# Optimization experiments

Measured on AMD Instinct MI355X. Metric: run time of the kernel, lower is better.

## Reference

```python
import jax, jax.numpy as jnp
import numpy as np

HEADS = 8
DIM_HEAD = 32
SCALE = DIM_HEAD ** -0.5


def setup_inputs() -> dict:
    key = jax.random.key(0)
    k1, k2, k3 = jax.random.split(key, 3)
    B, H, W, C = 16, 64, 64, 256
    hidden = HEADS * DIM_HEAD  # 256
    x = jax.random.normal(k1, (B, H, W, C), dtype=jnp.float32)
    # 1x1 convs with no bias == dense matmuls over channel dim (glorot-ish scale)
    w_qkv = jax.random.normal(k2, (C, 3 * hidden), dtype=jnp.float32) * (1.0 / np.sqrt(C))
    w_out = jax.random.normal(k3, (hidden, C), dtype=jnp.float32) * (1.0 / np.sqrt(hidden))
    return {"x": x, "w_qkv": w_qkv, "w_out": w_out}


def reference(x, w_qkv, w_out):
    B, H, W, C = x.shape
    n = H * W
    # to_qkv: 1x1 conv, no bias
    qkv = jnp.einsum('bhwc,cf->bhwf', x, w_qkv)  # [B,H,W,3*hidden]
    q, k, v = jnp.split(qkv, 3, axis=-1)

    def to_heads(t):
        # 'b x y (h c) -> b h c (x y)'
        t = t.reshape(B, n, HEADS, DIM_HEAD)
        return jnp.transpose(t, (0, 2, 3, 1))  # [B, heads, dim_head, n]

    q, k, v = to_heads(q), to_heads(k), to_heads(v)
    q = jax.nn.softmax(q, axis=-2) * SCALE      # softmax over feature dim d
    k = jax.nn.softmax(k, axis=-1)              # softmax over spatial dim n
    context = jnp.einsum('bhdn,bhen->bhde', k, v)   # [B, heads, d, e]
    out = jnp.einsum('bhde,bhdn->bhen', context, q)  # [B, heads, e, n]
    # 'b h c (x y) -> b x y (h c)'
    out = jnp.transpose(out, (0, 3, 1, 2)).reshape(B, H, W, HEADS * DIM_HEAD)
    # to_out: 1x1 conv, no bias
    return jnp.einsum('bhwf,fc->bhwc', out, w_out)
```

## Files before the change

kernel.cpp:

```cpp
#include <hip/hip_runtime.h>

using short8 = __attribute__((ext_vector_type(8))) short;
using f32x4  = __attribute__((ext_vector_type(4))) float;

#define SCALE_Q 0.17677669529663687f
#define NCHUNK 16

__device__ __forceinline__ unsigned short f2bf(float f) {
  unsigned u = __float_as_uint(f);
  return (unsigned short)((u + 0x7FFFu + ((u >> 16) & 1u)) >> 16);
}
__device__ __forceinline__ float bf2f(unsigned h) { return __uint_as_float(h << 16); }

__device__ __forceinline__ void bf8_to_f(uint4 r, float* o) {
  o[0] = bf2f(r.x & 0xffffu); o[1] = bf2f(r.x >> 16);
  o[2] = bf2f(r.y & 0xffffu); o[3] = bf2f(r.y >> 16);
  o[4] = bf2f(r.z & 0xffffu); o[5] = bf2f(r.z >> 16);
  o[6] = bf2f(r.w & 0xffffu); o[7] = bf2f(r.w >> 16);
}

__global__ __launch_bounds__(256) void prep_kernel(
    const float* __restrict__ x, const float* __restrict__ wqkv, const float* __restrict__ wout,
    unsigned short* __restrict__ xb, unsigned short* __restrict__ wqkvT,
    unsigned short* __restrict__ woutT) {
  const int blk = blockIdx.x;
  if (blk < 16384) {
    const size_t i = ((size_t)blk * 256 + threadIdx.x) * 4;
    const float4 v = *(const float4*)(x + i);
    *(ushort4*)(xb + i) = make_ushort4(f2bf(v.x), f2bf(v.y), f2bf(v.z), f2bf(v.w));
  } else if (blk < 16384 + 768) {
    const int n = blk - 16384, k = threadIdx.x;
    wqkvT[n * 256 + k] = f2bf(wqkv[(size_t)k * 768 + n]);
  } else {
    const int c = blk - 16384 - 768, f = threadIdx.x;
    woutT[c * 256 + f] = f2bf(wout[(size_t)f * 256 + c]);
  }
}

__global__ __launch_bounds__(256) void gemm_qkv(
    const unsigned short* __restrict__ A, const unsigned short* __restrict__ BT,
    unsigned short* __restrict__ KV, unsigned short* __restrict__ QS, int K) {
  __shared__ unsigned short As[2][128][40];
  __shared__ unsigned short Bs[2][128][40];
  const int cpx = (int)gridDim.x >> 3;
  const int lin = ((int)blockIdx.x & 7) * cpx + ((int)blockIdx.x >> 3);
  const int bn = lin % 6, bm = lin / 6;
  const int tid = threadIdx.x, lane = tid & 63, wid = tid >> 6;
  const int wr = wid >> 1, wc = wid & 1;
  const int fr = lane & 15, hi = lane >> 4, fk = hi * 8;
  f32x4 acc[4][4] = {};
  const size_t abase = (size_t)bm * 128 * K;
  const size_t bbase = (size_t)bn * 128 * K;

  const int srow = tid >> 2, skc = (tid & 3) * 8;
  uint4 ra0, ra1, rb0, rb1;
  const unsigned short* Ap = A + abase + (size_t)srow * K + skc;
  const unsigned short* Bp = BT + bbase + (size_t)srow * K + skc;

  ra0 = *(const uint4*)(Ap);            ra1 = *(const uint4*)(Ap + (size_t)64 * K);
  rb0 = *(const uint4*)(Bp);            rb1 = *(const uint4*)(Bp + (size_t)64 * K);
  *(uint4*)&As[0][srow][skc] = ra0;     *(uint4*)&As[0][srow + 64][skc] = ra1;
  *(uint4*)&Bs[0][srow][skc] = rb0;     *(uint4*)&Bs[0][srow + 64][skc] = rb1;
  __syncthreads();

  const int ktiles = K >> 5;
  int cur = 0;
  for (int t = 0; t < ktiles; ++t) {
    if (t + 1 < ktiles) {
      const int kt = (t + 1) * 32;
      ra0 = *(const uint4*)(Ap + kt);     ra1 = *(const uint4*)(Ap + (size_t)64 * K + kt);
      rb0 = *(const uint4*)(Bp + kt);     rb1 = *(const uint4*)(Bp + (size_t)64 * K + kt);
    }
    short8 af[4], bfv[4];
#pragma unroll
    for (int i = 0; i < 4; ++i) {
      af[i]  = *(const short8*)&As[cur][wr * 64 + i * 16 + fr][fk];
      bfv[i] = *(const short8*)&Bs[cur][wc * 64 + i * 16 + fr][fk];
    }
#pragma unroll
    for (int mi = 0; mi < 4; ++mi)
#pragma unroll
      for (int nj = 0; nj < 4; ++nj)
        acc[mi][nj] = __builtin_amdgcn_mfma_f32_16x16x32_bf16(bfv[nj], af[mi], acc[mi][nj], 0, 0, 0);
    if (t + 1 < ktiles) {
      *(uint4*)&As[cur ^ 1][srow][skc] = ra0;  *(uint4*)&As[cur ^ 1][srow + 64][skc] = ra1;
      *(uint4*)&Bs[cur ^ 1][srow][skc] = rb0;  *(uint4*)&Bs[cur ^ 1][srow + 64][skc] = rb1;
    }
    __syncthreads();
    cur ^= 1;
  }

  const size_t r0 = (size_t)bm * 128 + wr * 64;
  if (bn < 2) {
    const int c0 = bn * 128 + wc * 64;
#pragma unroll
    for (int mi = 0; mi < 4; ++mi) {
      const size_t row = r0 + mi * 16 + fr;
#pragma unroll
      for (int p = 0; p < 2; ++p) {
        const f32x4 a0 = acc[mi][2 * p], a1 = acc[mi][2 * p + 1];
        float mx = fmaxf(fmaxf(fmaxf(a0[0], a0[1]), fmaxf(a0[2], a0[3])),
                         fmaxf(fmaxf(a1[0], a1[1]), fmaxf(a1[2], a1[3])));
        mx = fmaxf(mx, __shfl_xor(mx, 16, 64));
        mx = fmaxf(mx, __shfl_xor(mx, 32, 64));
        float e0[4], e1[4], s = 0.f;
#pragma unroll
        for (int r = 0; r < 4; ++r) {
          e0[r] = __expf(a0[r] - mx); e1[r] = __expf(a1[r] - mx);
          s += e0[r] + e1[r];
        }
        s += __shfl_xor(s, 16, 64);
        s += __shfl_xor(s, 32, 64);
        const float inv = SCALE_Q / s;
        unsigned short* qp = QS + row * 256 + c0 + p * 32 + hi * 4;
        *(ushort4*)(qp)      = make_ushort4(f2bf(e0[0]*inv), f2bf(e0[1]*inv), f2bf(e0[2]*inv), f2bf(e0[3]*inv));
        *(ushort4*)(qp + 16) = make_ushort4(f2bf(e1[0]*inv), f2bf(e1[1]*inv), f2bf(e1[2]*inv), f2bf(e1[3]*inv));
      }
    }
    return;
  }
  const int colbase = (bn - 2) * 128 + wc * 64;
#pragma unroll
  for (int mi = 0; mi < 4; ++mi) {
    const size_t row = r0 + mi * 16 + fr;
#pragma unroll
    for (int nj = 0; nj < 4; ++nj) {
      const int col0 = colbase + nj * 16 + hi * 4;
      const f32x4 v = acc[mi][nj];
      *(ushort4*)(KV + row * 512 + col0) =
          make_ushort4(f2bf(v[0]), f2bf(v[1]), f2bf(v[2]), f2bf(v[3]));
    }
  }
}

__global__ __launch_bounds__(256) void gemm_out(
    const unsigned short* __restrict__ A, const unsigned short* __restrict__ BT,
    float* __restrict__ D, int K) {
  __shared__ unsigned short As[2][128][40];
  __shared__ unsigned short Bs[2][128][40];
  const int bn = blockIdx.x, bm = blockIdx.y, bz = blockIdx.z;
  const int tid = threadIdx.x, lane = tid & 63, wid = tid >> 6;
  const int wr = wid >> 1, wc = wid & 1;
  const int fr = lane & 15, hi = lane >> 4, fk = hi * 8;
  f32x4 acc[4][4] = {};
  const size_t abase = (size_t)bz * 4096 * 256 + (size_t)bm * 128 * K;
  const size_t bbase = (size_t)bz * 256 * 256 + (size_t)bn * 128 * K;

  const int srow = tid >> 2, skc = (tid & 3) * 8;
  uint4 ra0, ra1, rb0, rb1;
  const unsigned short* Ap = A + abase + (size_t)srow * K + skc;
  const unsigned short* Bp = BT + bbase + (size_t)srow * K + skc;

  ra0 = *(const uint4*)(Ap);            ra1 = *(const uint4*)(Ap + (size_t)64 * K);
  rb0 = *(const uint4*)(Bp);            rb1 = *(const uint4*)(Bp + (size_t)64 * K);
  *(uint4*)&As[0][srow][skc] = ra0;     *(uint4*)&As[0][srow + 64][skc] = ra1;
  *(uint4*)&Bs[0][srow][skc] = rb0;     *(uint4*)&Bs[0][srow + 64][skc] = rb1;
  __syncthreads();

  const int ktiles = K >> 5;
  int cur = 0;
  for (int t = 0; t < ktiles; ++t) {
    if (t + 1 < ktiles) {
      const int kt = (t + 1) * 32;
      ra0 = *(const uint4*)(Ap + kt);     ra1 = *(const uint4*)(Ap + (size_t)64 * K + kt);
      rb0 = *(const uint4*)(Bp + kt);     rb1 = *(const uint4*)(Bp + (size_t)64 * K + kt);
    }
    short8 af[4], bfv[4];
#pragma unroll
    for (int i = 0; i < 4; ++i) {
      af[i]  = *(const short8*)&As[cur][wr * 64 + i * 16 + fr][fk];
      bfv[i] = *(const short8*)&Bs[cur][wc * 64 + i * 16 + fr][fk];
    }
#pragma unroll
    for (int mi = 0; mi < 4; ++mi)
#pragma unroll
      for (int nj = 0; nj < 4; ++nj)
        acc[mi][nj] = __builtin_amdgcn_mfma_f32_16x16x32_bf16(bfv[nj], af[mi], acc[mi][nj], 0, 0, 0);
    if (t + 1 < ktiles) {
      *(uint4*)&As[cur ^ 1][srow][skc] = ra0;  *(uint4*)&As[cur ^ 1][srow + 64][skc] = ra1;
      *(uint4*)&Bs[cur ^ 1][srow][skc] = rb0;  *(uint4*)&Bs[cur ^ 1][srow + 64][skc] = rb1;
    }
    __syncthreads();
    cur ^= 1;
  }

  const size_t r0 = (size_t)bm * 128 + wr * 64;
  const int colbase = bn * 128 + wc * 64;
  float* Dz = D + (size_t)bz * 4096 * 256;
#pragma unroll
  for (int mi = 0; mi < 4; ++mi) {
    const size_t row = r0 + mi * 16 + fr;
#pragma unroll
    for (int nj = 0; nj < 4; ++nj) {
      const f32x4 v = acc[mi][nj];
      *(float4*)(Dz + row * 256 + colbase + nj * 16 + hi * 4) =
          make_float4(v[0], v[1], v[2], v[3]);
    }
  }
}

__global__ __launch_bounds__(256) void ctx_part_kernel(const unsigned short* __restrict__ kv,
                                                       float* __restrict__ part,
                                                       float* __restrict__ spart) {
  const int blk = blockIdx.x;
  const int bh = blk >> 4, chunk = blk & 15;
  const int b = bh >> 3, h = bh & 7;
  const int tid = threadIdx.x, d = tid & 31, g = tid >> 5;
  const unsigned short* kbase =
      kv + (size_t)b * 4096 * 512 + h * 32 + (size_t)chunk * 256 * 512;
  const unsigned short* vbase = kbase + 256;

  __shared__ float ek[64][36], vv[64][36];
  float a0 = 0.f, a1 = 0.f, a2 = 0.f, a3 = 0.f, ssum = 0.f;
  const int e0 = g * 4;
  const int sn = tid >> 2, sc = (tid & 3) * 8;
  const unsigned short* kp0 = kbase + (size_t)sn * 512 + sc;
  const unsigned short* vp0 = vbase + (size_t)sn * 512 + sc;
  uint4 kr = *(const uint4*)kp0;
  uint4 vr = *(const uint4*)vp0;
  for (int n0 = 0; n0 < 256; n0 += 64) {
    float kf[8], vf[8];
    bf8_to_f(kr, kf); bf8_to_f(vr, vf);
    uint4 krn = kr, vrn = vr;
    if (n0 + 64 < 256) {
      krn = *(const uint4*)(kp0 + (size_t)(n0 + 64) * 512);
      vrn = *(const uint4*)(vp0 + (size_t)(n0 + 64) * 512);
    }
#pragma unroll
    for (int j = 0; j < 8; ++j) { ek[sn][sc + j] = __expf(kf[j]); vv[sn][sc + j] = vf[j]; }
    __syncthreads();
#pragma unroll 8
    for (int i = 0; i < 64; ++i) {
      const float kd = ek[i][d];
      const float4 v4 = *(const float4*)&vv[i][e0];
      ssum += kd;
      a0 += kd * v4.x; a1 += kd * v4.y; a2 += kd * v4.z; a3 += kd * v4.w;
    }
    __syncthreads();
    kr = krn; vr = vrn;
  }
  float* pp = part + ((size_t)chunk * 128 + bh) * 1024 + d * 32 + e0;
  pp[0] = a0; pp[1] = a1; pp[2] = a2; pp[3] = a3;
  if (g == 0) spart[((size_t)chunk * 128 + bh) * 32 + d] = ssum;
}

__global__ __launch_bounds__(256) void ctx_combine_kernel(const float* __restrict__ part,
                                                          const float* __restrict__ spart,
                                                          float* __restrict__ ctx) {
  const int bh = blockIdx.x, tid = threadIdx.x;
  __shared__ float sinv[32];
  if (tid < 32) {
    float s = 0.f;
#pragma unroll
    for (int c = 0; c < NCHUNK; ++c) s += spart[((size_t)c * 128 + bh) * 32 + tid];
    sinv[tid] = 1.0f / s;
  }
  __syncthreads();
  float4 acc = make_float4(0.f, 0.f, 0.f, 0.f);
#pragma unroll
  for (int c = 0; c < NCHUNK; ++c) {
    const float4 p = *(const float4*)(part + ((size_t)c * 128 + bh) * 1024 + tid * 4);
    acc.x += p.x; acc.y += p.y; acc.z += p.z; acc.w += p.w;
  }
  const float si = sinv[tid >> 3];
  float4* cp = (float4*)(ctx + (size_t)bh * 1024 + tid * 4);
  *cp = make_float4(acc.x * si, acc.y * si, acc.z * si, acc.w * si);
}

__global__ __launch_bounds__(256) void w2_kernel(const float* __restrict__ ctx,
                                                 const unsigned short* __restrict__ woutT,
                                                 unsigned short* __restrict__ W2T) {
  const int b = blockIdx.x >> 4, cg = blockIdx.x & 15;
  const int tid = threadIdx.x;
  __shared__ float cs[8 * 32 * 32];
  {
    const float4* src = (const float4*)(ctx + (size_t)b * 8192);
    float4* dst = (float4*)cs;
#pragma unroll
    for (int i = 0; i < 8; ++i) dst[tid + i * 256] = src[tid + i * 256];
  }
  __syncthreads();
  const int c = cg * 16 + (tid >> 4), chunk = tid & 15;
  const int h = chunk >> 1, d0 = (chunk & 1) * 16;
  float wf[32];
  {
    const uint4* wp = (const uint4*)(woutT + (size_t)c * 256 + h * 32);
    bf8_to_f(wp[0], wf + 0); bf8_to_f(wp[1], wf + 8);
    bf8_to_f(wp[2], wf + 16); bf8_to_f(wp[3], wf + 24);
  }
  unsigned short o[16];
#pragma unroll
  for (int dd = 0; dd < 16; ++dd) {
    const float* cp = cs + h * 1024 + (d0 + dd) * 32;
    float acc = 0.f;
#pragma unroll
    for (int e = 0; e < 32; ++e) acc += cp[e] * wf[e];
    o[dd] = f2bf(acc);
  }
  uint4* op = (uint4*)(W2T + ((size_t)b * 256 + c) * 256 + chunk * 16);
  op[0] = make_uint4((unsigned)o[0] | ((unsigned)o[1] << 16), (unsigned)o[2] | ((unsigned)o[3] << 16),
                     (unsigned)o[4] | ((unsigned)o[5] << 16), (unsigned)o[6] | ((unsigned)o[7] << 16));
  op[1] = make_uint4((unsigned)o[8] | ((unsigned)o[9] << 16), (unsigned)o[10] | ((unsigned)o[11] << 16),
                     (unsigned)o[12] | ((unsigned)o[13] << 16), (unsigned)o[14] | ((unsigned)o[15] << 16));
}

extern "C" void kernel_launch(void* const* d_in, const int* in_sizes, int n_in,
                              void* d_out, int out_size, void* d_ws, size_t ws_size,
                              hipStream_t stream) {
  const float* x     = (const float*)d_in[0];
  const float* wqkv  = (const float*)d_in[1];
  const float* wout  = (const float*)d_in[2];
  float* out = (float*)d_out;

  char* ws = (char*)d_ws;
  unsigned short* xb    = (unsigned short*)(ws);
  unsigned short* wqkvT = (unsigned short*)(ws + 33554432);
  unsigned short* woutT = (unsigned short*)(ws + 33947648);
  unsigned short* kv    = (unsigned short*)(ws + 34078720);
  float*          ctx   = (float*)        (ws + 101187584);
  unsigned short* qs    = (unsigned short*)(ws + 101711872);
  float*          part  = (float*)(ws);
  float*          spart = (float*)(ws + 8388608);
  unsigned short* W2T   = (unsigned short*)(ws + 12582912);

  prep_kernel<<<16384 + 768 + 256, 256, 0, stream>>>(x, wqkv, wout, xb, wqkvT, woutT);
  gemm_qkv<<<3072, 256, 0, stream>>>(xb, wqkvT, kv, qs, 256);
  ctx_part_kernel<<<2048, 256, 0, stream>>>(kv, part, spart);
  ctx_combine_kernel<<<128, 256, 0, stream>>>(part, spart, ctx);
  w2_kernel<<<256, 256, 0, stream>>>(ctx, woutT, W2T);
  gemm_out<<<dim3(2, 32, 16), 256, 0, stream>>>(qs, W2T, out, 256);
}
```

Before: 159.5 us.

## Fuse x fp32-to-bf16 conversion into QKV GEMM and swizzle output GEMM grid

The separate pass that converted x to bf16 in the workspace is removed. The QKV GEMM now loads fp32 x directly and packs it to bf16 while staging into shared memory. This removes a 64MB read plus 32MB write round trip, at the cost of doubling A-operand global load bytes inside the GEMM, which re-reads x once for each of the 6 column tiles. It also switches bf16 packing to the paired hardware conversion intrinsic and gives gemm_out a 1D grid with an XCD-aware block remap.

```diff
diff --git a/kernel.cpp b/kernel.cpp
--- a/kernel.cpp
+++ b/kernel.cpp
@@ -1,4 +1,5 @@
 #include <hip/hip_runtime.h>
+#include <hip/hip_bf16.h>
 
 using short8 = __attribute__((ext_vector_type(8))) short;
 using f32x4  = __attribute__((ext_vector_type(4))) float;
@@ -11,6 +12,12 @@
   return (unsigned short)((u + 0x7FFFu + ((u >> 16) & 1u)) >> 16);
 }
 __device__ __forceinline__ float bf2f(unsigned h) { return __uint_as_float(h << 16); }
+
+__device__ __forceinline__ unsigned pk2(float a, float b) {
+  union { __hip_bfloat162 h; unsigned u; } cv;
+  cv.h = __float22bfloat162_rn(make_float2(a, b));
+  return cv.u;
+}
 
 __device__ __forceinline__ void bf8_to_f(uint4 r, float* o) {
   o[0] = bf2f(r.x & 0xffffu); o[1] = bf2f(r.x >> 16);
@@ -20,25 +27,20 @@
 }
 
 __global__ __launch_bounds__(256) void prep_kernel(
-    const float* __restrict__ x, const float* __restrict__ wqkv, const float* __restrict__ wout,
-    unsigned short* __restrict__ xb, unsigned short* __restrict__ wqkvT,
-    unsigned short* __restrict__ woutT) {
+    const float* __restrict__ wqkv, const float* __restrict__ wout,
+    unsigned short* __restrict__ wqkvT, unsigned short* __restrict__ woutT) {
   const int blk = blockIdx.x;
-  if (blk < 16384) {
-    const size_t i = ((size_t)blk * 256 + threadIdx.x) * 4;
-    const float4 v = *(const float4*)(x + i);
-    *(ushort4*)(xb + i) = make_ushort4(f2bf(v.x), f2bf(v.y), f2bf(v.z), f2bf(v.w));
-  } else if (blk < 16384 + 768) {
-    const int n = blk - 16384, k = threadIdx.x;
+  if (blk < 768) {
+    const int n = blk, k = threadIdx.x;
     wqkvT[n * 256 + k] = f2bf(wqkv[(size_t)k * 768 + n]);
   } else {
-    const int c = blk - 16384 - 768, f = threadIdx.x;
+    const int c = blk - 768, f = threadIdx.x;
     woutT[c * 256 + f] = f2bf(wout[(size_t)f * 256 + c]);
   }
 }
 
 __global__ __launch_bounds__(256) void gemm_qkv(
-    const unsigned short* __restrict__ A, const unsigned short* __restrict__ BT,
+    const float* __restrict__ X, const unsigned short* __restrict__ BT,
     unsigned short* __restrict__ KV, unsigned short* __restrict__ QS, int K) {
   __shared__ unsigned short As[2][128][40];
   __shared__ unsigned short Bs[2][128][40];
@@ -49,18 +51,20 @@
   const int wr = wid >> 1, wc = wid & 1;
   const int fr = lane & 15, hi = lane >> 4, fk = hi * 8;
   f32x4 acc[4][4] = {};
-  const size_t abase = (size_t)bm * 128 * K;
-  const size_t bbase = (size_t)bn * 128 * K;
 
   const int srow = tid >> 2, skc = (tid & 3) * 8;
-  uint4 ra0, ra1, rb0, rb1;
-  const unsigned short* Ap = A + abase + (size_t)srow * K + skc;
-  const unsigned short* Bp = BT + bbase + (size_t)srow * K + skc;
-
-  ra0 = *(const uint4*)(Ap);            ra1 = *(const uint4*)(Ap + (size_t)64 * K);
-  rb0 = *(const uint4*)(Bp);            rb1 = *(const uint4*)(Bp + (size_t)64 * K);
-  *(uint4*)&As[0][srow][skc] = ra0;     *(uint4*)&As[0][srow + 64][skc] = ra1;
-  *(uint4*)&Bs[0][srow][skc] = rb0;     *(uint4*)&Bs[0][srow + 64][skc] = rb1;
+  const float* Ap = X + (size_t)bm * 128 * K + (size_t)srow * K + skc;
+  const unsigned short* Bp = BT + (size_t)bn * 128 * K + (size_t)srow * K + skc;
+
+  float4 fa0, fa1, fa2, fa3; uint4 rb0, rb1;
+  fa0 = *(const float4*)(Ap);                       fa1 = *(const float4*)(Ap + 4);
+  fa2 = *(const float4*)(Ap + (size_t)64 * K);      fa3 = *(const float4*)(Ap + (size_t)64 * K + 4);
+  rb0 = *(const uint4*)(Bp);                        rb1 = *(const uint4*)(Bp + (size_t)64 * K);
+  *(uint4*)&As[0][srow][skc] =
+      make_uint4(pk2(fa0.x, fa0.y), pk2(fa0.z, fa0.w), pk2(fa1.x, fa1.y), pk2(fa1.z, fa1.w));
+  *(uint4*)&As[0][srow + 64][skc] =
+      make_uint4(pk2(fa2.x, fa2.y), pk2(fa2.z, fa2.w), pk2(fa3.x, fa3.y), pk2(fa3.z, fa3.w));
+  *(uint4*)&Bs[0][srow][skc] = rb0;                 *(uint4*)&Bs[0][srow + 64][skc] = rb1;
   __syncthreads();
 
   const int ktiles = K >> 5;
@@ -68,8 +72,9 @@
   for (int t = 0; t < ktiles; ++t) {
     if (t + 1 < ktiles) {
       const int kt = (t + 1) * 32;
-      ra0 = *(const uint4*)(Ap + kt);     ra1 = *(const uint4*)(Ap + (size_t)64 * K + kt);
-      rb0 = *(const uint4*)(Bp + kt);     rb1 = *(const uint4*)(Bp + (size_t)64 * K + kt);
+      fa0 = *(const float4*)(Ap + kt);                   fa1 = *(const float4*)(Ap + kt + 4);
+      fa2 = *(const float4*)(Ap + (size_t)64 * K + kt);  fa3 = *(const float4*)(Ap + (size_t)64 * K + kt + 4);
+      rb0 = *(const uint4*)(Bp + kt);                    rb1 = *(const uint4*)(Bp + (size_t)64 * K + kt);
     }
     short8 af[4], bfv[4];
 #pragma unroll
@@ -83,7 +88,10 @@
       for (int nj = 0; nj < 4; ++nj)
         acc[mi][nj] = __builtin_amdgcn_mfma_f32_16x16x32_bf16(bfv[nj], af[mi], acc[mi][nj], 0, 0, 0);
     if (t + 1 < ktiles) {
-      *(uint4*)&As[cur ^ 1][srow][skc] = ra0;  *(uint4*)&As[cur ^ 1][srow + 64][skc] = ra1;
+      *(uint4*)&As[cur ^ 1][srow][skc] =
+          make_uint4(pk2(fa0.x, fa0.y), pk2(fa0.z, fa0.w), pk2(fa1.x, fa1.y), pk2(fa1.z, fa1.w));
+      *(uint4*)&As[cur ^ 1][srow + 64][skc] =
+          make_uint4(pk2(fa2.x, fa2.y), pk2(fa2.z, fa2.w), pk2(fa3.x, fa3.y), pk2(fa3.z, fa3.w));
       *(uint4*)&Bs[cur ^ 1][srow][skc] = rb0;  *(uint4*)&Bs[cur ^ 1][srow + 64][skc] = rb1;
     }
     __syncthreads();
@@ -113,8 +121,8 @@
         s += __shfl_xor(s, 32, 64);
         const float inv = SCALE_Q / s;
         unsigned short* qp = QS + row * 256 + c0 + p * 32 + hi * 4;
-        *(ushort4*)(qp)      = make_ushort4(f2bf(e0[0]*inv), f2bf(e0[1]*inv), f2bf(e0[2]*inv), f2bf(e0[3]*inv));
-        *(ushort4*)(qp + 16) = make_ushort4(f2bf(e1[0]*inv), f2bf(e1[1]*inv), f2bf(e1[2]*inv), f2bf(e1[3]*inv));
+        *(uint2*)(qp)      = make_uint2(pk2(e0[0]*inv, e0[1]*inv), pk2(e0[2]*inv, e0[3]*inv));
+        *(uint2*)(qp + 16) = make_uint2(pk2(e1[0]*inv, e1[1]*inv), pk2(e1[2]*inv, e1[3]*inv));
       }
     }
     return;
@@ -127,8 +135,7 @@
     for (int nj = 0; nj < 4; ++nj) {
       const int col0 = colbase + nj * 16 + hi * 4;
       const f32x4 v = acc[mi][nj];
-      *(ushort4*)(KV + row * 512 + col0) =
-          make_ushort4(f2bf(v[0]), f2bf(v[1]), f2bf(v[2]), f2bf(v[3]));
+      *(uint2*)(KV + row * 512 + col0) = make_uint2(pk2(v[0], v[1]), pk2(v[2], v[3]));
     }
   }
 }
@@ -138,7 +145,9 @@
     float* __restrict__ D, int K) {
   __shared__ unsigned short As[2][128][40];
   __shared__ unsigned short Bs[2][128][40];
-  const int bn = blockIdx.x, bm = blockIdx.y, bz = blockIdx.z;
+  const int cpx = (int)gridDim.x >> 3;
+  const int lin = ((int)blockIdx.x & 7) * cpx + ((int)blockIdx.x >> 3);
+  const int bn = lin & 1, bm = (lin >> 1) & 31, bz = lin >> 6;
   const int tid = threadIdx.x, lane = tid & 63, wid = tid >> 6;
   const int wr = wid >> 1, wc = wid & 1;
   const int fr = lane & 15, hi = lane >> 4, fk = hi * 8;
@@ -313,20 +322,19 @@
   float* out = (float*)d_out;
 
   char* ws = (char*)d_ws;
-  unsigned short* xb    = (unsigned short*)(ws);
+  float*          part  = (float*)(ws);
+  float*          spart = (float*)(ws + 8388608);
+  unsigned short* W2T   = (unsigned short*)(ws + 12582912);
   unsigned short* wqkvT = (unsigned short*)(ws + 33554432);
   unsigned short* woutT = (unsigned short*)(ws + 33947648);
   unsigned short* kv    = (unsigned short*)(ws + 34078720);
   float*          ctx   = (float*)        (ws + 101187584);
   unsigned short* qs    = (unsigned short*)(ws + 101711872);
-  float*          part  = (float*)(ws);
-  float*          spart = (float*)(ws + 8388608);
-  unsigned short* W2T   = (unsigned short*)(ws + 12582912);
-
-  prep_kernel<<<16384 + 768 + 256, 256, 0, stream>>>(x, wqkv, wout, xb, wqkvT, woutT);
-  gemm_qkv<<<3072, 256, 0, stream>>>(xb, wqkvT, kv, qs, 256);
+
+  prep_kernel<<<1024, 256, 0, stream>>>(wqkv, wout, wqkvT, woutT);
+  gemm_qkv<<<3072, 256, 0, stream>>>(x, wqkvT, kv, qs, 256);
   ctx_part_kernel<<<2048, 256, 0, stream>>>(kv, part, spart);
   ctx_combine_kernel<<<128, 256, 0, stream>>>(part, spart, ctx);
   w2_kernel<<<256, 256, 0, stream>>>(ctx, woutT, W2T);
-  gemm_out<<<dim3(2, 32, 16), 256, 0, stream>>>(qs, W2T, out, 256);
-}
+  gemm_out<<<1024, 256, 0, stream>>>(qs, W2T, out, 256);
+}
```

Result: faster. 152.6 us (-4.3%).
